# Performance work log

Measured on AMD Instinct MI355X. Metric: run time of the kernel, lower is better.

The kernel has to match this reference:

```python
import jax, jax.numpy as jnp
import numpy as np

D = 256          # d_model
H = 8            # decoder_attention_heads
HD = D // H      # attn_feat_dim = 32
L = 4            # num_feature_levels
P = 4            # decoder_n_points
B = 32           # batch
NQ = 100         # num_queries
T_SHAPES = [2048, 1024, 512, 256]   # temporal length per feature level
T_TOTAL = sum(T_SHAPES)


def setup_inputs() -> dict:
    key = jax.random.key(0)
    ks = jax.random.split(key, 16)
    rn = lambda k, s, sc=1.0: jax.random.normal(k, s, jnp.float32) * sc
    w = 0.02
    inp = {}
    inp['token'] = rn(ks[0], (B * NQ, D))
    inp['h0'] = rn(ks[1], (1, B * NQ, D))
    inp['c0'] = rn(ks[2], (1, B * NQ, D))
    inp['query'] = rn(ks[3], (B, NQ, D))
    inp['reference_points'] = jax.random.uniform(ks[4], (B, NQ, L, 1), jnp.float32)
    inp['encoder_hidden_states'] = rn(ks[5], (B, T_TOTAL, D))
    inp['mask_flatten'] = jnp.zeros((B, T_TOTAL), bool)   # True = padded
    inp['temporal_shapes'] = jnp.array(T_SHAPES, jnp.int32)
    # TemporalMSDA params (offsets/weights act on concat(prev_h, query) -> 2*D)
    inp['W_value'] = rn(ks[6], (D, D), w);      inp['b_value'] = jnp.zeros((D,), jnp.float32)
    inp['W_off'] = rn(ks[7], (2 * D, H * L * P), w); inp['b_off'] = rn(ks[8], (H * L * P,), w)
    inp['W_aw'] = rn(ks[9], (2 * D, H * L * P), w);  inp['b_aw'] = jnp.zeros((H * L * P,), jnp.float32)
    # additive attention params
    inp['W_ctx'] = rn(ks[10], (HD, D), w);  inp['b_ctx'] = jnp.zeros((D,), jnp.float32)
    inp['W_hs'] = rn(ks[11], (D, D), w);    inp['b_hs'] = jnp.zeros((D,), jnp.float32)
    inp['W_alpha'] = rn(ks[12], (D, 1), w); inp['b_alpha'] = jnp.zeros((1,), jnp.float32)
    # LSTM (bias=False), gate order i,f,g,o
    inp['W_ih'] = rn(ks[13], (4 * D, 3 * D), w)
    inp['W_hh'] = rn(ks[14], (4 * D, D), w)
    return inp


def _deformable_sample(value, reference_points, off, aw):
    """Per-point sampled values weighted by MSDA attention weights.
    value: (B,T,H,HD); off: (B,NQ,H,L,P); aw: (B,NQ,H,L,P) -> (B*NQ,H,L*P,HD)"""
    starts = np.concatenate([[0], np.cumsum(T_SHAPES)[:-1]])
    sampled = []
    for l in range(L):
        Tl = T_SHAPES[l]
        v_l = value[:, starts[l]:starts[l] + Tl].transpose(0, 2, 1, 3)  # (B,H,Tl,HD)
        # normalized sampling location in [0,1]
        loc = reference_points[:, :, None, l, :] + off[:, :, :, l, :] / Tl  # (B,NQ,H,P)
        x = loc * Tl - 0.5                      # align_corners=False grid
        x0 = jnp.floor(x)
        w1 = x - x0
        w0 = 1.0 - w1
        i0 = x0.astype(jnp.int32)
        i1 = i0 + 1
        m0 = ((i0 >= 0) & (i0 < Tl)).astype(value.dtype)   # zero padding outside
        m1 = ((i1 >= 0) & (i1 < Tl)).astype(value.dtype)
        idx0 = jnp.clip(i0, 0, Tl - 1).transpose(0, 2, 1, 3).reshape(B, H, NQ * P)
        idx1 = jnp.clip(i1, 0, Tl - 1).transpose(0, 2, 1, 3).reshape(B, H, NQ * P)
        g0 = jnp.take_along_axis(v_l, idx0[..., None], axis=2).reshape(B, H, NQ, P, HD)
        g1 = jnp.take_along_axis(v_l, idx1[..., None], axis=2).reshape(B, H, NQ, P, HD)
        w0t = (w0 * m0).transpose(0, 2, 1, 3)[..., None]   # (B,H,NQ,P,1)
        w1t = (w1 * m1).transpose(0, 2, 1, 3)[..., None]
        sampled.append(g0 * w0t + g1 * w1t)                # (B,H,NQ,P,HD)
    samp = jnp.stack(sampled, axis=3)                      # (B,H,NQ,L,P,HD)
    awt = aw.transpose(0, 2, 1, 3, 4)[..., None]           # (B,H,NQ,L,P,1)
    feats = (samp * awt).reshape(B, H, NQ, L * P, HD)
    return feats.transpose(0, 2, 1, 3, 4).reshape(B * NQ, H, L * P, HD)


def reference(token, h0, c0, query, reference_points, encoder_hidden_states,
              mask_flatten, temporal_shapes,
              W_value, b_value, W_off, b_off, W_aw, b_aw,
              W_ctx, b_ctx, W_hs, b_hs, W_alpha, b_alpha, W_ih, W_hh):
    prev_h = h0[-1]                                        # (B*NQ, D)
    hs = jnp.concatenate([prev_h.reshape(B, NQ, D), query], axis=-1)  # (B,NQ,2D)

    # TemporalMSDA (is_captioning=True -> per-point weighted samples)
    value = encoder_hidden_states @ W_value + b_value
    value = jnp.where(mask_flatten[:, :, None], 0.0, value).reshape(B, T_TOTAL, H, HD)
    off = (hs @ W_off + b_off).reshape(B, NQ, H, L, P)
    aw = jax.nn.softmax((hs @ W_aw + b_aw).reshape(B, NQ, H, L * P), axis=-1)
    aw = aw.reshape(B, NQ, H, L, P)
    feats = _deformable_sample(value, reference_points, off, aw)  # (B*NQ,H,LP,HD)

    # dual-linear additive attention over the L*P sampled points
    attn = jnp.tanh(jnp.einsum('nhpd,de->nhpe', feats, W_ctx) + b_ctx
                    + (prev_h @ W_hs + b_hs)[:, None, None, :])    # (B*NQ,H,LP,D)
    scores = jnp.einsum('nhpe,eo->nhpo', attn, W_alpha)[..., 0] + b_alpha[0]
    weight = jax.nn.softmax(scores, axis=-1)                       # (B*NQ,H,LP)
    attn_res = jnp.einsum('nhp,nhpd->nhd', weight, feats).reshape(B * NQ, D)

    # single LSTM step, bias=False, gate order i,f,g,o
    x = jnp.concatenate([token, attn_res, query.reshape(B * NQ, D)], axis=-1)
    gates = x @ W_ih.T + prev_h @ W_hh.T
    i, f, g, o = jnp.split(gates, 4, axis=-1)
    c_new = jax.nn.sigmoid(f) * c0[-1] + jax.nn.sigmoid(i) * jnp.tanh(g)
    h_new = jax.nn.sigmoid(o) * jnp.tanh(c_new)
    return h_new, h_new[None], c_new[None]
```

## Files before the change

### kernel.cpp

```cpp
#include <hip/hip_runtime.h>
#include <math.h>

#define NB   32
#define NQn  100
#define NN   3200
#define DM   256
#define NH   8
#define HDd  32
#define TT   3840

typedef __attribute__((ext_vector_type(8))) short bf16x8;
typedef __attribute__((ext_vector_type(4))) float f32x4;

__device__ __forceinline__ float fast_tanh(float x) {
    float t = __expf(2.0f * x);
    return 1.0f - 2.0f * __builtin_amdgcn_rcpf(t + 1.0f);
}
__device__ __forceinline__ float fast_sigmoid(float x) {
    return __builtin_amdgcn_rcpf(1.0f + __expf(-x));
}
__device__ __forceinline__ unsigned short f2b(float f) {
    unsigned u = __float_as_uint(f);
    unsigned r = u + 0x7FFF + ((u >> 16) & 1);
    return (unsigned short)(r >> 16);
}
__device__ __forceinline__ float b2f(unsigned short h) {
    return __uint_as_float((unsigned)h << 16);
}
__device__ __forceinline__ unsigned pack2_trunc(float lo, float hi) {
    return __builtin_amdgcn_perm(__float_as_uint(hi), __float_as_uint(lo), 0x07060302u);
}

__global__ __launch_bounds__(256) void k0_prep(const float* __restrict__ Wih,
                                               const float* __restrict__ Whh,
                                               const float* __restrict__ Wctx,
                                               const float* __restrict__ Wv,
                                               const float* __restrict__ Woff,
                                               const float* __restrict__ Waw,
                                               const float* __restrict__ Whs,
                                               unsigned short* __restrict__ Wcatfrag,
                                               unsigned short* __restrict__ Wvfrag,
                                               unsigned short* __restrict__ Wfragb,
                                               unsigned short* __restrict__ Wk1frag) {
    int bid = blockIdx.x;
    int tid = threadIdx.x;
    if (bid < 256) {
        int cb = bid >> 2, q8 = bid & 3;
#pragma unroll
        for (int t2 = 0; t2 < 2; ++t2) {
            int idx = tid + t2 * 256;
            int s = q8 * 8 + (idx >> 6);
            int lane = idx & 63;
            int col = cb * 16 + (lane & 15);
            int kb = s * 32 + (lane >> 4) * 8;
            float vv[8];
            if (kb < 768) {
#pragma unroll
                for (int j = 0; j < 8; ++j) vv[j] = Wih[col * 768 + kb + j];
            } else {
#pragma unroll
                for (int j = 0; j < 8; ++j) vv[j] = Whh[col * 256 + (kb - 768) + j];
            }
            uint4 w;
            w.x = (unsigned)f2b(vv[0]) | ((unsigned)f2b(vv[1]) << 16);
            w.y = (unsigned)f2b(vv[2]) | ((unsigned)f2b(vv[3]) << 16);
            w.z = (unsigned)f2b(vv[4]) | ((unsigned)f2b(vv[5]) << 16);
            w.w = (unsigned)f2b(vv[6]) | ((unsigned)f2b(vv[7]) << 16);
            *(uint4*)&Wcatfrag[(((cb * 32) + s) * 64 + lane) * 8] = w;
        }
    } else if (bid < 272) {
        int cb = bid - 256;
#pragma unroll
        for (int t2 = 0; t2 < 2; ++t2) {
            int idx = tid + t2 * 256;
            int s = idx >> 6;
            int lane = idx & 63;
            int n = cb * 16 + (lane & 15);
            int kb = s * 32 + (lane >> 4) * 8;
            float vv[8];
#pragma unroll
            for (int j = 0; j < 8; ++j) vv[j] = Wv[(kb + j) * 256 + n];
            uint4 w;
            w.x = (unsigned)f2b(vv[0]) | ((unsigned)f2b(vv[1]) << 16);
            w.y = (unsigned)f2b(vv[2]) | ((unsigned)f2b(vv[3]) << 16);
            w.z = (unsigned)f2b(vv[4]) | ((unsigned)f2b(vv[5]) << 16);
            w.w = (unsigned)f2b(vv[6]) | ((unsigned)f2b(vv[7]) << 16);
            *(uint4*)&Wvfrag[(((cb * 8) + s) * 64 + lane) * 8] = w;
        }
    } else if (bid == 272) {
#pragma unroll
        for (int s4 = 0; s4 < 4; ++s4) {
            int slot = tid * 4 + s4;
            int et = slot >> 6, lane = slot & 63;
            int e = et * 16 + (lane & 15);
            int kb = (lane >> 4) * 8;
            unsigned short o[8];
#pragma unroll
            for (int j = 0; j < 8; ++j) o[j] = f2b(Wctx[(kb + j) * 256 + e]);
            *(uint4*)&Wfragb[slot * 8] = *(uint4*)o;
        }
    } else {
        int cb = bid - 273;
#pragma unroll
        for (int t4 = 0; t4 < 4; ++t4) {
            int idx = tid + t4 * 256;
            int s = idx >> 6, lane = idx & 63;
            int col = cb * 16 + (lane & 15);
            int kb = s * 32 + (lane >> 4) * 8;
            float vv[8];
            if (cb < 8) {
#pragma unroll
                for (int j = 0; j < 8; ++j) vv[j] = Woff[(kb + j) * 128 + col];
            } else if (cb < 16) {
#pragma unroll
                for (int j = 0; j < 8; ++j) vv[j] = Waw[(kb + j) * 128 + (col - 128)];
            } else if (kb < 256) {
#pragma unroll
                for (int j = 0; j < 8; ++j) vv[j] = Whs[(kb + j) * 256 + (col - 256)];
            } else {
#pragma unroll
                for (int j = 0; j < 8; ++j) vv[j] = 0.0f;
            }
            uint4 w;
            w.x = (unsigned)f2b(vv[0]) | ((unsigned)f2b(vv[1]) << 16);
            w.y = (unsigned)f2b(vv[2]) | ((unsigned)f2b(vv[3]) << 16);
            w.z = (unsigned)f2b(vv[4]) | ((unsigned)f2b(vv[5]) << 16);
            w.w = (unsigned)f2b(vv[6]) | ((unsigned)f2b(vv[7]) << 16);
            *(uint4*)&Wk1frag[(((cb * 16) + s) * 64 + lane) * 8] = w;
        }
    }
}

__global__ __launch_bounds__(256) void k1_proj(const float* __restrict__ h0,
                                               const float* __restrict__ query,
                                               const unsigned short* __restrict__ Wk1frag,
                                               const float* __restrict__ boff,
                                               const float* __restrict__ baw,
                                               const float* __restrict__ bhs,
                                               float* __restrict__ offb,
                                               float* __restrict__ awb,
                                               float* __restrict__ hsbb) {
    __shared__ __align__(16) unsigned short als[8192];
    __shared__ float awl[16][132];
    int tid = threadIdx.x;
    int n0 = blockIdx.x * 16;
    int y  = blockIdx.y;

#pragma unroll
    for (int i = 0; i < 4; ++i) {
        int r  = (tid & 7) + 8 * (i & 1);
        int kg = (tid >> 3) + 32 * (i >> 1);
        const float* base = (i >> 1) ? query : h0;
        const float* p = base + (size_t)(n0 + r) * 256 + (kg & 31) * 8;
        float4 u = *(const float4*)p;
        float4 v = *(const float4*)(p + 4);
        int s = kg >> 2, q = kg & 3;
        uint4 w;
        w.x = (unsigned)f2b(u.x) | ((unsigned)f2b(u.y) << 16);
        w.y = (unsigned)f2b(u.z) | ((unsigned)f2b(u.w) << 16);
        w.z = (unsigned)f2b(v.x) | ((unsigned)f2b(v.y) << 16);
        w.w = (unsigned)f2b(v.z) | ((unsigned)f2b(v.w) << 16);
        *(uint4*)&als[((s * 64) + (r & 15) + 16 * q) * 8] = w;
    }
    __syncthreads();

    int w = tid >> 6, lane = tid & 63;
    int l16 = lane & 15, quad = lane >> 4;
    int smax = (y >= 2) ? 8 : 16;

    f32x4 acc[2];
    f32x4 zero = {0.f, 0.f, 0.f, 0.f};
    acc[0] = zero; acc[1] = zero;

#pragma unroll 8
    for (int s = 0; s < smax; ++s) {
        bf16x8 a = *(bf16x8*)&als[(s * 64 + lane) * 8];
#pragma unroll
        for (int ct = 0; ct < 2; ++ct) {
            int cb = y * 8 + w * 2 + ct;
            bf16x8 bfr = *(const bf16x8*)&Wk1frag[(((cb * 16) + s) * 64 + lane) * 8];
            acc[ct] = __builtin_amdgcn_mfma_f32_16x16x32_bf16(a, bfr, acc[ct], 0, 0, 0);
        }
    }

    if (y == 0) {
#pragma unroll
        for (int ct = 0; ct < 2; ++ct) {
            int col = w * 32 + ct * 16 + l16;
            float bo = boff[col];
#pragma unroll
            for (int reg = 0; reg < 4; ++reg)
                offb[(size_t)(n0 + quad * 4 + reg) * 128 + col] = acc[ct][reg] + bo;
        }
    } else if (y == 1) {
#pragma unroll
        for (int ct = 0; ct < 2; ++ct) {
            int col = w * 32 + ct * 16 + l16;
            float ba = baw[col];
#pragma unroll
            for (int reg = 0; reg < 4; ++reg)
                awl[quad * 4 + reg][col] = acc[ct][reg] + ba;
        }
        __syncthreads();
        if (tid < 128) {
            int r = tid >> 3, h = tid & 7;
            float s[16];
            float mx = -1e30f;
#pragma unroll
            for (int i = 0; i < 16; ++i) {
                s[i] = awl[r][h * 16 + i];
                mx = fmaxf(mx, s[i]);
            }
            float sum = 0.f;
#pragma unroll
            for (int i = 0; i < 16; ++i) { s[i] = __expf(s[i] - mx); sum += s[i]; }
            float inv = 1.0f / sum;
#pragma unroll
            for (int i = 0; i < 16; ++i)
                awb[(size_t)(n0 + r) * 128 + h * 16 + i] = s[i] * inv;
        }
    } else {
#pragma unroll
        for (int ct = 0; ct < 2; ++ct) {
            int colh = (y - 2) * 128 + w * 32 + ct * 16 + l16;
            float bh = bhs[colh];
#pragma unroll
            for (int reg = 0; reg < 4; ++reg)
                hsbb[(size_t)(n0 + quad * 4 + reg) * 256 + colh] = acc[ct][reg] + bh;
        }
    }
}

__global__ __launch_bounds__(256) void k2_value(const float* __restrict__ eh,
                                                const unsigned short* __restrict__ Wvfrag,
                                                const float* __restrict__ bv,
                                                unsigned short* __restrict__ valueb) {
    __shared__ __align__(16) unsigned short lt[4][32 * 132];
    int tid = threadIdx.x;
    int w = tid >> 6, lane = tid & 63;
    int l16 = lane & 15, quad = lane >> 4;
    int wr = w & 1, wc = w >> 1;
    int m0 = blockIdx.x * 64 + wr * 32;
    int colbase = wc * 128;

    f32x4 acc[2][8];
    f32x4 zero = {0.f, 0.f, 0.f, 0.f};
#pragma unroll
    for (int mt = 0; mt < 2; ++mt)
#pragma unroll
        for (int nt = 0; nt < 8; ++nt) acc[mt][nt] = zero;

#pragma unroll
    for (int s = 0; s < 8; ++s) {
        union { bf16x8 v; unsigned u[4]; } a[2];
#pragma unroll
        for (int mt = 0; mt < 2; ++mt) {
            const float* p = eh + (size_t)(m0 + mt * 16 + l16) * 256 + s * 32 + quad * 8;
            float4 u = *(const float4*)p;
            float4 v = *(const float4*)(p + 4);
            a[mt].u[0] = pack2_trunc(u.x, u.y);
            a[mt].u[1] = pack2_trunc(u.z, u.w);
            a[mt].u[2] = pack2_trunc(v.x, v.y);
            a[mt].u[3] = pack2_trunc(v.z, v.w);
        }
#pragma unroll
        for (int nt = 0; nt < 8; ++nt) {
            int cb = wc * 8 + nt;
            bf16x8 bfr = *(const bf16x8*)&Wvfrag[(((cb * 8) + s) * 64 + lane) * 8];
            acc[0][nt] = __builtin_amdgcn_mfma_f32_16x16x32_bf16(a[0].v, bfr, acc[0][nt], 0, 0, 0);
            acc[1][nt] = __builtin_amdgcn_mfma_f32_16x16x32_bf16(a[1].v, bfr, acc[1][nt], 0, 0, 0);
        }
    }

    unsigned short* myl = lt[w];
#pragma unroll
    for (int nt = 0; nt < 8; ++nt) {
        float bvv = bv[colbase + nt * 16 + l16];
#pragma unroll
        for (int mt = 0; mt < 2; ++mt) {
#pragma unroll
            for (int reg = 0; reg < 4; ++reg) {
                int rl = mt * 16 + quad * 4 + reg;
                myl[rl * 132 + nt * 16 + l16] = f2b(acc[mt][nt][reg] + bvv);
            }
        }
    }
    __syncthreads();
#pragma unroll
    for (int i = 0; i < 8; ++i) {
        int idx = i * 64 + lane;
        int lr = idx >> 4, c16 = idx & 15;
        *(uint4*)&valueb[(size_t)(m0 + lr) * 256 + colbase + c16 * 8] =
            *(uint4*)&myl[lr * 132 + c16 * 8];
    }
}

__global__ __launch_bounds__(256) void k3_attn(const float* __restrict__ rp,
                                               const float* __restrict__ offb,
                                               const float* __restrict__ awb,
                                               const float* __restrict__ hsbb,
                                               const unsigned short* __restrict__ valueb,
                                               const unsigned short* __restrict__ Wfragb,
                                               const float* __restrict__ bctx,
                                               const float* __restrict__ walpha,
                                               float* __restrict__ attnres) {
    __shared__ __align__(16) unsigned short featsb[128 * 40];
    __shared__ float hb[256];
    __shared__ float wa[256];
    __shared__ float scores[128];
    __shared__ float weight[8][16];

    int n = blockIdx.x;
    int b = n / NQn;
    int tid = threadIdx.x;

    {
        int pair = tid >> 1;
        int dh = (tid & 1) * 16;
        int h = pair >> 4;
        int lp = pair & 15;
        int l = lp >> 2;
        int Tli = 2048 >> l;
        int st = 4096 - (4096 >> l);
        float Tlf = (float)Tli;
        float invT = __uint_as_float((unsigned)(127 - (11 - l)) << 23);

        float r = rp[n * 4 + l];
        float off_v = offb[n * 128 + pair];
        float aw_v = awb[n * 128 + pair];
        float loc = r + off_v * invT;
        float x = loc * Tlf - 0.5f;
        float x0 = floorf(x);
        float w1 = x - x0;
        float w0 = 1.0f - w1;
        int i0 = (int)x0;
        int i1 = i0 + 1;
        float m0 = (i0 >= 0 && i0 < Tli) ? 1.0f : 0.0f;
        float m1 = (i1 >= 0 && i1 < Tli) ? 1.0f : 0.0f;
        int idx0 = min(max(i0, 0), Tli - 1);
        int idx1 = min(max(i1, 0), Tli - 1);
        float a0 = w0 * m0 * aw_v;
        float a1 = w1 * m1 * aw_v;
        const unsigned short* g0 = valueb + (size_t)(b * TT + st + idx0) * 256 + h * 32 + dh;
        const unsigned short* g1 = valueb + (size_t)(b * TT + st + idx1) * 256 + h * 32 + dh;
        union U8 { uint4 u; unsigned short s[8]; };
        U8 A0, A1, B0, B1;
        A0.u = *(const uint4*)g0;  A1.u = *(const uint4*)(g0 + 8);
        B0.u = *(const uint4*)g1;  B1.u = *(const uint4*)(g1 + 8);
        unsigned short o[16];
#pragma unroll
        for (int i = 0; i < 8; ++i) {
            o[i]     = f2b(b2f(A0.s[i]) * a0 + b2f(B0.s[i]) * a1);
            o[8 + i] = f2b(b2f(A1.s[i]) * a0 + b2f(B1.s[i]) * a1);
        }
        *(uint4*)&featsb[pair * 40 + dh]     = *(uint4*)&o[0];
        *(uint4*)&featsb[pair * 40 + dh + 8] = *(uint4*)&o[8];
    }
    hb[tid] = bctx[tid] + hsbb[n * 256 + tid];
    wa[tid] = walpha[tid];
    __syncthreads();

    {
        int w = tid >> 6, lane = tid & 63;
        int l16 = lane & 15, quad = lane >> 4;
        bf16x8 a0 = *(bf16x8*)&featsb[(w * 32 + l16) * 40 + quad * 8];
        bf16x8 a1 = *(bf16x8*)&featsb[(w * 32 + 16 + l16) * 40 + quad * 8];
        f32x4 zero = {0.f, 0.f, 0.f, 0.f};
        float sc0[4] = {0.f, 0.f, 0.f, 0.f};
        float sc1[4] = {0.f, 0.f, 0.f, 0.f};
#pragma unroll
        for (int et = 0; et < 16; ++et) {
            bf16x8 bfr = *(const bf16x8*)&Wfragb[(et * 64 + lane) * 8];
            float hbv = hb[et * 16 + l16];
            float wav = wa[et * 16 + l16];
            f32x4 z0 = __builtin_amdgcn_mfma_f32_16x16x32_bf16(a0, bfr, zero, 0, 0, 0);
            f32x4 z1 = __builtin_amdgcn_mfma_f32_16x16x32_bf16(a1, bfr, zero, 0, 0, 0);
#pragma unroll
            for (int reg = 0; reg < 4; ++reg) {
                sc0[reg] += wav * fast_tanh(z0[reg] + hbv);
                sc1[reg] += wav * fast_tanh(z1[reg] + hbv);
            }
        }
#pragma unroll
        for (int off = 1; off < 16; off <<= 1) {
#pragma unroll
            for (int reg = 0; reg < 4; ++reg) {
                sc0[reg] += __shfl_xor(sc0[reg], off);
                sc1[reg] += __shfl_xor(sc1[reg], off);
            }
        }
        if (l16 == 0) {
#pragma unroll
            for (int reg = 0; reg < 4; ++reg) {
                scores[w * 32 + quad * 4 + reg]      = sc0[reg];
                scores[w * 32 + 16 + quad * 4 + reg] = sc1[reg];
            }
        }
    }
    __syncthreads();

    if (tid < 8) {
        int h = tid;
        float s[16];
        float mx = -1e30f;
#pragma unroll
        for (int i = 0; i < 16; ++i) {
            s[i] = scores[h * 16 + i];
            mx = fmaxf(mx, s[i]);
        }
        float sum = 0.f;
#pragma unroll
        for (int i = 0; i < 16; ++i) { s[i] = __expf(s[i] - mx); sum += s[i]; }
        float inv = 1.0f / sum;
#pragma unroll
        for (int i = 0; i < 16; ++i) weight[h][i] = s[i] * inv;
    }
    __syncthreads();

    {
        int h = tid >> 5, d = tid & 31;
        float s = 0.f;
#pragma unroll
        for (int lp = 0; lp < 16; ++lp)
            s += weight[h][lp] * b2f(featsb[(h * 16 + lp) * 40 + d]);
        attnres[n * 256 + tid] = s;
    }
}

__global__ __launch_bounds__(256) void k4_lstm(const float* __restrict__ token,
                                               const float* __restrict__ attnres,
                                               const float* __restrict__ query,
                                               const float* __restrict__ h0,
                                               const unsigned short* __restrict__ Wcatfrag,
                                               const float* __restrict__ c0,
                                               float* __restrict__ out) {
    __shared__ __align__(16) unsigned short lds[16384];
    int tid = threadIdx.x;
    int n0 = blockIdx.x * 16;
    int j0 = blockIdx.y * 64;

    const float* const srcs[4] = {token, attnres, query, h0};
#pragma unroll
    for (int i = 0; i < 8; ++i) {
        int c = i >> 1;
        int r = (tid & 7) + 8 * (i & 1);
        int kgl = tid >> 3;
        const float* p = srcs[c] + (size_t)(n0 + r) * 256 + kgl * 8;
        float4 u = *(const float4*)p;
        float4 v = *(const float4*)(p + 4);
        int s = c * 8 + (kgl >> 2), q = kgl & 3;
        uint4 w;
        w.x = (unsigned)f2b(u.x) | ((unsigned)f2b(u.y) << 16);
        w.y = (unsigned)f2b(u.z) | ((unsigned)f2b(u.w) << 16);
        w.z = (unsigned)f2b(v.x) | ((unsigned)f2b(v.y) << 16);
        w.w = (unsigned)f2b(v.z) | ((unsigned)f2b(v.w) << 16);
        *(uint4*)&lds[((s * 64) + r + 16 * q) * 8] = w;
    }
    __syncthreads();

    int w = tid >> 6, lane = tid & 63;
    int l16 = lane & 15, quad = lane >> 4;
    int cbbase = (j0 >> 4) + w;

    f32x4 acc[4];
    f32x4 zero = {0.f, 0.f, 0.f, 0.f};
#pragma unroll
    for (int seg = 0; seg < 4; ++seg) acc[seg] = zero;

#pragma unroll 4
    for (int s = 0; s < 32; ++s) {
        bf16x8 a = *(bf16x8*)&lds[(s * 64 + lane) * 8];
#pragma unroll
        for (int seg = 0; seg < 4; ++seg) {
            bf16x8 bfr = *(const bf16x8*)&Wcatfrag[((((seg * 16 + cbbase) * 32) + s) * 64 + lane) * 8];
            acc[seg] = __builtin_amdgcn_mfma_f32_16x16x32_bf16(a, bfr, acc[seg], 0, 0, 0);
        }
    }

    int colg = j0 + w * 16 + l16;
#pragma unroll
    for (int reg = 0; reg < 4; ++reg) {
        int row = n0 + quad * 4 + reg;
        float gi = acc[0][reg];
        float gf = acc[1][reg];
        float gg = acc[2][reg];
        float go = acc[3][reg];
        float c0v = c0[row * 256 + colg];
        float cn = fast_sigmoid(gf) * c0v + fast_sigmoid(gi) * fast_tanh(gg);
        float hn = fast_sigmoid(go) * fast_tanh(cn);
        int o = row * 256 + colg;
        out[o] = hn;
        out[NN * 256 + o] = hn;
        out[2 * NN * 256 + o] = cn;
    }
}

extern "C" void kernel_launch(void* const* d_in, const int* in_sizes, int n_in,
                              void* d_out, int out_size, void* d_ws, size_t ws_size,
                              hipStream_t stream) {
    (void)in_sizes; (void)n_in; (void)out_size; (void)ws_size;
    const float* token = (const float*)d_in[0];
    const float* h0    = (const float*)d_in[1];
    const float* c0    = (const float*)d_in[2];
    const float* query = (const float*)d_in[3];
    const float* rp    = (const float*)d_in[4];
    const float* eh    = (const float*)d_in[5];
    const float* Wv   = (const float*)d_in[8];
    const float* bv   = (const float*)d_in[9];
    const float* Woff = (const float*)d_in[10];
    const float* boff = (const float*)d_in[11];
    const float* Waw  = (const float*)d_in[12];
    const float* baw  = (const float*)d_in[13];
    const float* Wctx = (const float*)d_in[14];
    const float* bctx = (const float*)d_in[15];
    const float* Whs  = (const float*)d_in[16];
    const float* bhs  = (const float*)d_in[17];
    const float* Wal  = (const float*)d_in[18];
    const float* Wih  = (const float*)d_in[20];
    const float* Whh  = (const float*)d_in[21];
    float* out = (float*)d_out;

    char* ws = (char*)d_ws;
    unsigned short* valueb   = (unsigned short*)(ws);
    unsigned short* Wcatfrag = (unsigned short*)(ws + 62914560);
    unsigned short* Wvfrag   = (unsigned short*)(ws + 65011712);
    unsigned short* Wfragb   = (unsigned short*)(ws + 65142784);
    float* offb    = (float*)(ws + 65159168);
    float* awb     = (float*)(ws + 66797568);
    float* hsbb    = (float*)(ws + 68435968);
    float* attnres = (float*)(ws + 71712768);
    unsigned short* Wk1frag  = (unsigned short*)(ws + 74989568);

    k0_prep<<<305, 256, 0, stream>>>(Wih, Whh, Wctx, Wv, Woff, Waw, Whs,
                                     Wcatfrag, Wvfrag, Wfragb, Wk1frag);
    k1_proj<<<dim3(NN / 16, 4), 256, 0, stream>>>(h0, query, Wk1frag, boff, baw, bhs,
                                                  offb, awb, hsbb);
    k2_value<<<(NB * TT) / 64, 256, 0, stream>>>(eh, Wvfrag, bv, valueb);
    k3_attn<<<NN, 256, 0, stream>>>(rp, offb, awb, hsbb, valueb, Wfragb, bctx, Wal, attnres);
    k4_lstm<<<dim3(NN / 16, 4), 256, 0, stream>>>(token, attnres, query, h0, Wcatfrag, c0, out);
}
```

Before: 383.9 us.

## Split value projection into bf16 conversion pass and full-width MFMA GEMM

Adds a separate kernel that converts encoder hidden states from fp32 to bf16 into a workspace buffer. The value GEMM then reads bf16 rows, with each wave computing 16 rows across all 256 columns. Previously each row was loaded as fp32 and converted by two column-split waves. This removes the duplicated fp32 reads and in-loop conversion, at the cost of an extra launch and a round trip of the bf16 copy through global memory.

New measurement: 465.8 us. 1.21x slower.

```diff
diff --git a/kernel.cpp b/kernel.cpp
--- a/kernel.cpp
+++ b/kernel.cpp
@@ -231,67 +231,63 @@
     }
 }
 
-__global__ __launch_bounds__(256) void k2_value(const float* __restrict__ eh,
-                                                const unsigned short* __restrict__ Wvfrag,
-                                                const float* __restrict__ bv,
-                                                unsigned short* __restrict__ valueb) {
-    __shared__ __align__(16) unsigned short lt[4][32 * 132];
+__global__ __launch_bounds__(256) void k2a_cvt(const float* __restrict__ eh,
+                                               unsigned short* __restrict__ ehb) {
+    int tid = threadIdx.x;
+    size_t base = (size_t)blockIdx.x * 8192;
+#pragma unroll
+    for (int it = 0; it < 4; ++it) {
+        size_t off = base + (size_t)(it * 256 + tid) * 8;
+        float4 u = *(const float4*)&eh[off];
+        float4 v = *(const float4*)&eh[off + 4];
+        uint4 w;
+        w.x = pack2_trunc(u.x, u.y);
+        w.y = pack2_trunc(u.z, u.w);
+        w.z = pack2_trunc(v.x, v.y);
+        w.w = pack2_trunc(v.z, v.w);
+        *(uint4*)&ehb[off] = w;
+    }
+}
+
+__global__ __launch_bounds__(256) void k2b_value(const unsigned short* __restrict__ ehb,
+                                                 const unsigned short* __restrict__ Wvfrag,
+                                                 const float* __restrict__ bv,
+                                                 unsigned short* __restrict__ valueb) {
+    __shared__ __align__(16) unsigned short lt[4][16 * 264];
     int tid = threadIdx.x;
     int w = tid >> 6, lane = tid & 63;
     int l16 = lane & 15, quad = lane >> 4;
-    int wr = w & 1, wc = w >> 1;
-    int m0 = blockIdx.x * 64 + wr * 32;
-    int colbase = wc * 128;
-
-    f32x4 acc[2][8];
+    int m0 = blockIdx.x * 64 + w * 16;
+
+    f32x4 acc[16];
     f32x4 zero = {0.f, 0.f, 0.f, 0.f};
 #pragma unroll
-    for (int mt = 0; mt < 2; ++mt)
-#pragma unroll
-        for (int nt = 0; nt < 8; ++nt) acc[mt][nt] = zero;
+    for (int nt = 0; nt < 16; ++nt) acc[nt] = zero;
 
 #pragma unroll
     for (int s = 0; s < 8; ++s) {
-        union { bf16x8 v; unsigned u[4]; } a[2];
-#pragma unroll
-        for (int mt = 0; mt < 2; ++mt) {
-            const float* p = eh + (size_t)(m0 + mt * 16 + l16) * 256 + s * 32 + quad * 8;
-            float4 u = *(const float4*)p;
-            float4 v = *(const float4*)(p + 4);
-            a[mt].u[0] = pack2_trunc(u.x, u.y);
-            a[mt].u[1] = pack2_trunc(u.z, u.w);
-            a[mt].u[2] = pack2_trunc(v.x, v.y);
-            a[mt].u[3] = pack2_trunc(v.z, v.w);
-        }
-#pragma unroll
-        for (int nt = 0; nt < 8; ++nt) {
-            int cb = wc * 8 + nt;
-            bf16x8 bfr = *(const bf16x8*)&Wvfrag[(((cb * 8) + s) * 64 + lane) * 8];
-            acc[0][nt] = __builtin_amdgcn_mfma_f32_16x16x32_bf16(a[0].v, bfr, acc[0][nt], 0, 0, 0);
-            acc[1][nt] = __builtin_amdgcn_mfma_f32_16x16x32_bf16(a[1].v, bfr, acc[1][nt], 0, 0, 0);
+        bf16x8 a = *(const bf16x8*)&ehb[(size_t)(m0 + l16) * 256 + s * 32 + quad * 8];
+#pragma unroll
+        for (int nt = 0; nt < 16; ++nt) {
+            bf16x8 bfr = *(const bf16x8*)&Wvfrag[(((nt * 8) + s) * 64 + lane) * 8];
+            acc[nt] = __builtin_amdgcn_mfma_f32_16x16x32_bf16(a, bfr, acc[nt], 0, 0, 0);
         }
     }
 
     unsigned short* myl = lt[w];
 #pragma unroll
-    for (int nt = 0; nt < 8; ++nt) {
-        float bvv = bv[colbase + nt * 16 + l16];
-#pragma unroll
-        for (int mt = 0; mt < 2; ++mt) {
-#pragma unroll
-            for (int reg = 0; reg < 4; ++reg) {
-                int rl = mt * 16 + quad * 4 + reg;
-                myl[rl * 132 + nt * 16 + l16] = f2b(acc[mt][nt][reg] + bvv);
-            }
-        }
+    for (int nt = 0; nt < 16; ++nt) {
+        float bvv = bv[nt * 16 + l16];
+#pragma unroll
+        for (int reg = 0; reg < 4; ++reg)
+            myl[(quad * 4 + reg) * 264 + nt * 16 + l16] = f2b(acc[nt][reg] + bvv);
     }
     __syncthreads();
 #pragma unroll
     for (int i = 0; i < 8; ++i) {
         int idx = i * 64 + lane;
-        int lr = idx >> 4, c16 = idx & 15;
-        *(uint4*)&valueb[(size_t)(m0 + lr) * 256 + colbase + c16 * 8] =
-            *(uint4*)&myl[lr * 132 + c16 * 8];
+        int lr = idx >> 5, c = idx & 31;
+        *(uint4*)&valueb[(size_t)(m0 + lr) * 256 + c * 8] = *(uint4*)&myl[lr * 264 + c * 8];
     }
 }
 
@@ -530,12 +526,14 @@
     float* hsbb    = (float*)(ws + 68435968);
     float* attnres = (float*)(ws + 71712768);
     unsigned short* Wk1frag  = (unsigned short*)(ws + 74989568);
+    unsigned short* ehb      = (unsigned short*)(ws + 76038144);
 
     k0_prep<<<305, 256, 0, stream>>>(Wih, Whh, Wctx, Wv, Woff, Waw, Whs,
                                      Wcatfrag, Wvfrag, Wfragb, Wk1frag);
     k1_proj<<<dim3(NN / 16, 4), 256, 0, stream>>>(h0, query, Wk1frag, boff, baw, bhs,
                                                   offb, awb, hsbb);
-    k2_value<<<(NB * TT) / 64, 256, 0, stream>>>(eh, Wvfrag, bv, valueb);
+    k2a_cvt<<<3840, 256, 0, stream>>>(eh, ehb);
+    k2b_value<<<(NB * TT) / 64, 256, 0, stream>>>(ehb, Wvfrag, bv, valueb);
     k3_attn<<<NN, 256, 0, stream>>>(rp, offb, awb, hsbb, valueb, Wfragb, bctx, Wal, attnres);
     k4_lstm<<<dim3(NN / 16, 4), 256, 0, stream>>>(token, attnres, query, h0, Wcatfrag, c0, out);
 }
```
